# Performance work log

Hardware: AMD Instinct MI355X
Metric: run time of the kernel (lower is better)

The kernel has to match this reference:

```python
import jax, jax.numpy as jnp
import numpy as np

_OFF = [(dz, dy, dx) for dz in (-1, 0, 1) for dy in (-1, 0, 1) for dx in (-1, 0, 1)]
_K3 = [(kz, ky, kx) for kz in range(3) for ky in range(3) for kx in range(3)]


def _key(c, dims):
    D, H, W = dims
    return ((c[:, 0].astype(np.int64) * D + c[:, 1]) * H + c[:, 2]) * W + c[:, 3]


def _dedupe(c, dims):
    k = _key(c, dims)
    _, idx = np.unique(k, return_index=True)
    return c[np.sort(idx)]


def _make_lookup(coords, dims):
    D, H, W = dims
    keys = _key(coords, dims)
    order = np.argsort(keys)
    skeys = keys[order]

    def query(qc):
        valid = ((qc[:, 1] >= 0) & (qc[:, 1] < D) & (qc[:, 2] >= 0) & (qc[:, 2] < H)
                 & (qc[:, 3] >= 0) & (qc[:, 3] < W))
        qk = _key(np.where(valid[:, None], qc, 0), dims)
        pos = np.clip(np.searchsorted(skeys, qk), 0, len(skeys) - 1)
        hit = valid & (skeys[pos] == qk)
        return np.where(hit, order[pos], -1).astype(np.int32)
    return query


def _subm_nbr(coords, query):
    nbr = np.empty((len(coords), 27), np.int32)
    for ki, (dz, dy, dx) in enumerate(_OFF):
        qc = coords.copy()
        qc[:, 1] += dz; qc[:, 2] += dy; qc[:, 3] += dx
        nbr[:, ki] = query(qc)
    return nbr


def _down(in_coords, pads, out_dims, in_query):
    # spconv SparseConv3d k=3 s=2: output active set + gather rulebook (in = 2*out - p + k)
    p = np.array(pads)
    cand = []
    for k in _K3:
        t = in_coords[:, 1:] + p - np.array(k)
        m = (t % 2 == 0).all(1)
        o = t[m] // 2
        ok = (o >= 0).all(1) & (o < np.array(out_dims)).all(1)
        cand.append(np.concatenate([in_coords[m][ok][:, :1], o[ok]], 1))
    out_coords = _dedupe(np.concatenate(cand), out_dims)
    nbrd = np.empty((len(out_coords), 27), np.int32)
    for ki, k in enumerate(_K3):
        qc = out_coords.copy()
        qc[:, 1:] = out_coords[:, 1:] * 2 - p + np.array(k)
        nbrd[:, ki] = in_query(qc)
    return out_coords, nbrd


def _inv(in_coords, pads, out_query):
    # inverse conv: for each stride-s input voxel i, gather downsampled voxel o = (i+p-k)/2
    p = np.array(pads)
    nbr = np.full((len(in_coords), 27), -1, np.int32)
    for ki, k in enumerate(_K3):
        t = in_coords[:, 1:] + p - np.array(k)
        div = (t % 2 == 0).all(1)
        qc = in_coords.copy()
        qc[:, 1:] = np.where(div[:, None], t // 2, -1)
        nbr[:, ki] = np.where(div, out_query(qc), -1)
    return nbr


def setup_inputs() -> dict:
    rng = np.random.default_rng(0)
    B, K, P, STD = 4, 160, 128, 3.0
    D1 = (41, 1024, 1024)  # sparse_shape (z, y, x)
    pts = []
    for b in range(B):
        ctr = np.stack([rng.uniform(2, d - 3, K) for d in D1], 1)
        pb = ctr[:, None, :] + rng.normal(0.0, STD, (K, P, 3))
        pb = np.clip(np.rint(pb.reshape(-1, 3)), 0, np.array(D1) - 1).astype(np.int64)
        pts.append(np.concatenate([np.full((len(pb), 1), b, np.int64), pb], 1))
    c1 = _dedupe(np.concatenate(pts), D1)
    D2 = tuple((d + 2 * q - 3) // 2 + 1 for d, q in zip(D1, (1, 1, 1)))
    D3 = tuple((d + 2 * q - 3) // 2 + 1 for d, q in zip(D2, (1, 1, 1)))
    D4 = tuple((d + 2 * q - 3) // 2 + 1 for d, q in zip(D3, (0, 1, 1)))
    q1 = _make_lookup(c1, D1); nbr1 = _subm_nbr(c1, q1)
    c2, nbrd2 = _down(c1, (1, 1, 1), D2, q1); q2 = _make_lookup(c2, D2); nbr2 = _subm_nbr(c2, q2)
    c3, nbrd3 = _down(c2, (1, 1, 1), D3, q2); q3 = _make_lookup(c3, D3); nbr3 = _subm_nbr(c3, q3)
    c4, nbrd4 = _down(c3, (0, 1, 1), D4, q3); q4 = _make_lookup(c4, D4); nbr4 = _subm_nbr(c4, q4)
    nbri4 = _inv(c3, (0, 1, 1), q4)
    nbri3 = _inv(c2, (1, 1, 1), q3)
    nbri2 = _inv(c1, (1, 1, 1), q2)
    N1 = len(c1)
    w = lambda *s: jnp.asarray((0.05 * rng.standard_normal(s)).astype(np.float32))
    bn = lambda n, c: jnp.asarray(np.stack([1.0 + 0.02 * rng.standard_normal((n, c)),
                                            0.02 * rng.standard_normal((n, c))], 1).astype(np.float32))
    return {
        'voxel_feat': jnp.asarray(rng.standard_normal((N1, 4)).astype(np.float32)),
        'Win': w(27, 4, 32),
        'W32': w(10, 27, 32, 32),
        'W64': w(10, 27, 64, 64),
        'Wd3': w(27, 32, 64),
        'W6432': w(3, 27, 64, 32),
        'W12864': w(2, 27, 128, 64),
        'bn32': bn(14, 32),
        'bn64': bn(13, 64),
        'nbr1': jnp.asarray(nbr1), 'nbr2': jnp.asarray(nbr2),
        'nbr3': jnp.asarray(nbr3), 'nbr4': jnp.asarray(nbr4),
        'nbrd2': jnp.asarray(nbrd2), 'nbrd3': jnp.asarray(nbrd3), 'nbrd4': jnp.asarray(nbrd4),
        'nbri4': jnp.asarray(nbri4), 'nbri3': jnp.asarray(nbri3), 'nbri2': jnp.asarray(nbri2),
    }


def _conv(feat, nbr, W):
    # rulebook gather-matmul-scatter: out[n] = sum_k feat[nbr[n,k]] @ W[k]
    out = jnp.zeros((nbr.shape[0], W.shape[-1]), feat.dtype)
    for k in range(27):
        idx = nbr[:, k]
        g = jnp.where((idx >= 0)[:, None], feat[jnp.maximum(idx, 0)], 0.0)
        out = out + g @ W[k]
    return out


def _block(f, nbr, W, sb):  # conv + (folded, eval-mode) BN + ReLU
    return jax.nn.relu(_conv(f, nbr, W) * sb[0] + sb[1])


def _basic(f, nbr, Wa, sa, Wb, sb):  # SparseBasicBlock
    h = jax.nn.relu(_conv(f, nbr, Wa) * sa[0] + sa[1])
    h = _conv(h, nbr, Wb) * sb[0] + sb[1]
    return jax.nn.relu(h + f)


def _reduce(c, oc):  # channel_reduction: view(n, oc, -1).sum(2)
    return c.reshape(c.shape[0], oc, -1).sum(-1)


def _forward(voxel_feat, Win, W32, W64, Wd3, W6432, W12864, bn32, bn64,
             nbr1, nbr2, nbr3, nbr4, nbrd2, nbrd3, nbrd4, nbri4, nbri3, nbri2):
    x = _block(voxel_feat, nbr1, Win, bn32[0])       # conv_input
    x1 = _block(x, nbr1, W32[0], bn32[1])            # conv1
    h = _block(x1, nbrd2, W32[1], bn32[2])           # spconv2 stride-2
    h = _block(h, nbr2, W32[2], bn32[3])
    x2 = _block(h, nbr2, W32[3], bn32[4])
    h = _block(x2, nbrd3, Wd3, bn64[0])              # spconv3 stride-2, 32->64
    h = _block(h, nbr3, W64[0], bn64[1])
    x3 = _block(h, nbr3, W64[1], bn64[2])
    h = _block(x3, nbrd4, W64[2], bn64[3])           # spconv4 stride-2, pad (0,1,1)
    h = _block(h, nbr4, W64[3], bn64[4])
    x4 = _block(h, nbr4, W64[4], bn64[5])
    # UR block 4 (lateral = bottom = x4)
    t = _basic(x4, nbr4, W64[5], bn64[6], W64[6], bn64[7])
    cat = jnp.concatenate([x4, t], 1)                # [N4, 128]
    x = _block(cat, nbr4, W12864[0], bn64[11]) + _reduce(cat, 64)
    xu4 = _block(x, nbri4, W64[7], bn64[8])          # inverseconv -> level 3
    # UR block 3
    t = _basic(x3, nbr3, W64[8], bn64[9], W64[9], bn64[10])
    cat = jnp.concatenate([xu4, t], 1)
    x = _block(cat, nbr3, W12864[1], bn64[12]) + _reduce(cat, 64)
    xu3 = _block(x, nbri3, W6432[0], bn32[11])       # inverseconv -> level 2, 32ch
    # UR block 2
    t = _basic(x2, nbr2, W32[4], bn32[5], W32[5], bn32[6])
    cat = jnp.concatenate([xu3, t], 1)
    x = _block(cat, nbr2, W6432[1], bn32[12]) + _reduce(cat, 32)
    xu2 = _block(x, nbri2, W32[6], bn32[7])          # inverseconv -> level 1
    # UR block 1 (conv_inv = conv5, submanifold at level 1)
    t = _basic(x1, nbr1, W32[7], bn32[8], W32[8], bn32[9])
    cat = jnp.concatenate([xu2, t], 1)
    x = _block(cat, nbr1, W6432[2], bn32[13]) + _reduce(cat, 32)
    return _block(x, nbr1, W32[9], bn32[10])         # conv5 -> unet_voxel_feat [N1, 32]


def reference(voxel_feat, Win, W32, W64, Wd3, W6432, W12864, bn32, bn64,
              nbr1, nbr2, nbr3, nbr4, nbrd2, nbrd3, nbrd4, nbri4, nbri3, nbri2):
    return _forward(voxel_feat, Win, W32, W64, Wd3, W6432, W12864, bn32, bn64,
                    nbr1, nbr2, nbr3, nbr4, nbrd2, nbrd3, nbrd4, nbri4, nbri3, nbri2)
```

## Files before the change

kernel.cpp:

```cpp
#include <hip/hip_runtime.h>


typedef float f32x16 __attribute__((ext_vector_type(16)));

template<int CIN_A, int CIN_B, int COUT, int EPI, bool SPLIT>
__global__ __launch_bounds__(256) void spconv(
    const float* __restrict__ inA,
    const float* __restrict__ inB,
    const int*   __restrict__ nbr,
    const float* __restrict__ W,
    const float* __restrict__ bn,
    const float* __restrict__ skip,
    float*       __restrict__ out,
    float*       __restrict__ pout,
    int N, int KS)
{
    constexpr int CIN   = CIN_A + CIN_B;
    constexpr int CHUNK = (CIN >= 32) ? 32 : CIN;
    constexpr int NCHK  = CIN / CHUNK;
    constexpr int GV    = CHUNK / 4;
    constexpr int NSTEP = CHUNK * COUT / 64;

    const int tid = threadIdx.x;

    unsigned nwg = gridDim.x;
    unsigned q8 = nwg / 8u, r8 = nwg % 8u;
    unsigned xcd = blockIdx.x % 8u, sub = blockIdx.x / 8u;
    unsigned id = (xcd < r8 ? xcd * (q8 + 1u) : r8 * (q8 + 1u) + (xcd - r8) * q8) + sub;

    int kg, rb;
    if (SPLIT) { kg = (int)(id % (unsigned)KS); rb = (int)(id / (unsigned)KS); }
    else       { kg = 0;  rb = (int)id; }
    const int kper = SPLIT ? 27 / KS : 27;
    const int k0 = kg * kper, k1 = k0 + kper;

    const int  row = rb * 256 + tid;
    const bool rv  = row < N;
    const int* nbrp = nbr + (size_t)row * 27;

    float acc[COUT];
    #pragma unroll
    for (int i = 0; i < COUT; ++i) acc[i] = 0.f;

    int idx = rv ? nbrp[k0] : -1;
    for (int k = k0; k < k1; ++k) {
        const int nidx = (rv && k + 1 < k1) ? nbrp[k + 1] : -1;
        if (__ballot(idx >= 0) != 0ull) {
            const float mk = (idx >= 0) ? 1.f : 0.f;
            const int   si = (idx >= 0) ? idx : 0;
            const float* wk = W + (size_t)k * (CIN * COUT);

            #pragma unroll 1
            for (int c = 0; c < NCHK; ++c) {
                const float* src;
                if constexpr (CIN_B == 0)
                    src = inA + (size_t)si * CIN_A + c * CHUNK;
                else
                    src = (c * CHUNK < CIN_A)
                        ? inA + (size_t)si * CIN_A + c * CHUNK
                        : inB + (size_t)si * CIN_B + (c * CHUNK - CIN_A);
                float4 g[GV];
                #pragma unroll
                for (int v = 0; v < GV; ++v) g[v] = ((const float4*)src)[v];
                #pragma unroll
                for (int v = 0; v < GV; ++v) {
                    g[v].x *= mk; g[v].y *= mk; g[v].z *= mk; g[v].w *= mk;
                }

                const float* wkc = wk + c * (CHUNK * COUT);
                #pragma unroll
                for (int ss = 0; ss < NSTEP; ++ss) {
                    const float* wp = wkc + ss * 64;
                    f32x16 w0, w1, w2, w3;
                    asm volatile("s_load_dwordx16 %0, %1, 0x0"  : "=s"(w0) : "s"(wp));
                    asm volatile("s_load_dwordx16 %0, %1, 0x40" : "=s"(w1) : "s"(wp));
                    asm volatile("s_load_dwordx16 %0, %1, 0x80" : "=s"(w2) : "s"(wp));
                    asm volatile("s_load_dwordx16 %0, %1, 0xc0" : "=s"(w3) : "s"(wp));
                    asm volatile("s_waitcnt lgkmcnt(0)"
                                 : "+s"(w0), "+s"(w1), "+s"(w2), "+s"(w3));
                    if constexpr (COUT == 64) {
                        const int ci = ss;
                        const float gv = ((const float*)&g[ci >> 2])[ci & 3];
                        #pragma unroll
                        for (int q = 0; q < 16; ++q) acc[q]      += gv * w0[q];
                        #pragma unroll
                        for (int q = 0; q < 16; ++q) acc[16 + q] += gv * w1[q];
                        #pragma unroll
                        for (int q = 0; q < 16; ++q) acc[32 + q] += gv * w2[q];
                        #pragma unroll
                        for (int q = 0; q < 16; ++q) acc[48 + q] += gv * w3[q];
                    } else {
                        const int ci0 = 2 * ss, ci1 = 2 * ss + 1;
                        const float gv0 = ((const float*)&g[ci0 >> 2])[ci0 & 3];
                        const float gv1 = ((const float*)&g[ci1 >> 2])[ci1 & 3];
                        #pragma unroll
                        for (int q = 0; q < 16; ++q) acc[q]      += gv0 * w0[q];
                        #pragma unroll
                        for (int q = 0; q < 16; ++q) acc[16 + q] += gv0 * w1[q];
                        #pragma unroll
                        for (int q = 0; q < 16; ++q) acc[q]      += gv1 * w2[q];
                        #pragma unroll
                        for (int q = 0; q < 16; ++q) acc[16 + q] += gv1 * w3[q];
                    }
                }
            }
        }
        idx = nidx;
    }

    if (SPLIT) {
        if (rv) {
            float* pp = pout + ((size_t)kg * N + row) * COUT;
            #pragma unroll
            for (int q = 0; q < COUT / 4; ++q)
                *(float4*)(pp + q * 4) = make_float4(acc[4*q], acc[4*q+1], acc[4*q+2], acc[4*q+3]);
        }
        return;
    }
    if (!rv) return;

    float*       op   = out + (size_t)row * COUT;
    const float* skp  = (EPI == 1) ? skip + (size_t)row * COUT : nullptr;
    const float* catA = inA + (size_t)row * CIN_A;
    const float* catB = (CIN_B > 0) ? inB + (size_t)row * CIN_B : nullptr;

    #pragma unroll
    for (int q = 0; q < COUT / 4; ++q) {
        float4 sc = *(const float4*)(bn + q * 4);
        float4 bi = *(const float4*)(bn + COUT + q * 4);
        float4 y;
        y.x = acc[4*q+0] * sc.x + bi.x;
        y.y = acc[4*q+1] * sc.y + bi.y;
        y.z = acc[4*q+2] * sc.z + bi.z;
        y.w = acc[4*q+3] * sc.w + bi.w;
        if (EPI == 1) {
            float4 s = *(const float4*)(skp + q * 4);
            y.x += s.x; y.y += s.y; y.z += s.z; y.w += s.w;
        }
        y.x = fmaxf(y.x, 0.f); y.y = fmaxf(y.y, 0.f);
        y.z = fmaxf(y.z, 0.f); y.w = fmaxf(y.w, 0.f);
        if (EPI == 2) {
            const float* rs = (8 * q < CIN_A) ? catA + 8 * q : catB + 8 * q - CIN_A;
            float4 p0 = ((const float4*)rs)[0];
            float4 p1 = ((const float4*)rs)[1];
            y.x += p0.x + p0.y; y.y += p0.z + p0.w;
            y.z += p1.x + p1.y; y.w += p1.z + p1.w;
        }
        *(float4*)(op + q * 4) = y;
    }
}

template<int CIN_A, int CIN_B, int COUT, int EPI>
__global__ __launch_bounds__(256) void epi_k(
    const float* __restrict__ P, int KS,
    const float* __restrict__ bn,
    const float* __restrict__ skip,
    const float* __restrict__ inA,
    const float* __restrict__ inB,
    float* __restrict__ out, int N)
{
    int t = blockIdx.x * 256 + threadIdx.x;
    int total = N * (COUT / 4);
    if (t >= total) return;
    int r   = t / (COUT / 4);
    int co0 = (t % (COUT / 4)) * 4;

    float4 y = make_float4(0.f, 0.f, 0.f, 0.f);
    for (int kg = 0; kg < KS; ++kg) {
        float4 p = *(const float4*)(P + ((size_t)kg * N + r) * COUT + co0);
        y.x += p.x; y.y += p.y; y.z += p.z; y.w += p.w;
    }
    float4 sc = *(const float4*)(bn + co0);
    float4 bi = *(const float4*)(bn + COUT + co0);
    y.x = y.x * sc.x + bi.x; y.y = y.y * sc.y + bi.y;
    y.z = y.z * sc.z + bi.z; y.w = y.w * sc.w + bi.w;
    if (EPI == 1) {
        float4 s = *(const float4*)(skip + (size_t)r * COUT + co0);
        y.x += s.x; y.y += s.y; y.z += s.z; y.w += s.w;
    }
    y.x = fmaxf(y.x, 0.f); y.y = fmaxf(y.y, 0.f);
    y.z = fmaxf(y.z, 0.f); y.w = fmaxf(y.w, 0.f);
    if (EPI == 2) {
        const float* rs = (2 * co0 < CIN_A)
            ? inA + (size_t)r * CIN_A + 2 * co0
            : inB + (size_t)r * CIN_B + 2 * co0 - CIN_A;
        float4 p0 = ((const float4*)rs)[0];
        float4 p1 = ((const float4*)rs)[1];
        y.x += p0.x + p0.y; y.y += p0.z + p0.w;
        y.z += p1.x + p1.y; y.w += p1.z + p1.w;
    }
    *(float4*)(out + (size_t)r * COUT + co0) = y;
}

static inline int ksel(int nblk, int N, int CO, size_t prem_elems) {
    int ks = 27;
    if (nblk >= 640) ks = 1;
    else if (nblk * 3 >= 640) ks = 3;
    else if (nblk * 9 >= 640) ks = 9;
    while (ks > 1 && (size_t)ks * (size_t)N * (size_t)CO > prem_elems) ks /= 3;
    return ks;
}

extern "C" void kernel_launch(void* const* d_in, const int* in_sizes, int n_in,
                              void* d_out, int out_size, void* d_ws, size_t ws_size,
                              hipStream_t stream)
{
    (void)n_in; (void)out_size;
    const float* vf     = (const float*)d_in[0];
    const float* Win    = (const float*)d_in[1];
    const float* W32    = (const float*)d_in[2];
    const float* W64    = (const float*)d_in[3];
    const float* Wd3    = (const float*)d_in[4];
    const float* W6432  = (const float*)d_in[5];
    const float* W12864 = (const float*)d_in[6];
    const float* bn32   = (const float*)d_in[7];
    const float* bn64   = (const float*)d_in[8];
    const int* nbr1  = (const int*)d_in[9];
    const int* nbr2  = (const int*)d_in[10];
    const int* nbr3  = (const int*)d_in[11];
    const int* nbr4  = (const int*)d_in[12];
    const int* nbrd2 = (const int*)d_in[13];
    const int* nbrd3 = (const int*)d_in[14];
    const int* nbrd4 = (const int*)d_in[15];
    const int* nbri4 = (const int*)d_in[16];
    const int* nbri3 = (const int*)d_in[17];
    const int* nbri2 = (const int*)d_in[18];

    const int N1 = in_sizes[9]  / 27;
    const int N2 = in_sizes[10] / 27;
    const int N3 = in_sizes[11] / 27;
    const int N4 = in_sizes[12] / 27;

    float* ws = (float*)d_ws;
    size_t off = 0;
    auto alloc = [&](size_t n) { float* p = ws + off; off += n; return p; };
    float* X1  = alloc((size_t)N1 * 32);
    float* TA  = alloc((size_t)N1 * 32);
    float* TA2 = alloc((size_t)N1 * 32);
    float* TU1 = alloc((size_t)N1 * 32);
    float* X2  = alloc((size_t)N2 * 32);
    float* TB2 = alloc((size_t)N2 * 32);
    float* TC2 = alloc((size_t)N2 * 32);
    float* TU2 = alloc((size_t)N2 * 32);
    float* X3  = alloc((size_t)N3 * 64);
    float* TB3 = alloc((size_t)N3 * 64);
    float* TC3 = alloc((size_t)N3 * 64);
    float* TU3 = alloc((size_t)N3 * 64);
    float* X4  = alloc((size_t)N4 * 64);
    float* TB4 = alloc((size_t)N4 * 64);
    float* TC4 = alloc((size_t)N4 * 64);
    float* OUT = (float*)d_out;

    size_t prem = (ws_size / 4 > off + 1024) ? (ws_size / 4 - off - 1024) : 0;
    float* P = ws + off;

    const size_t S32 = 27*32*32, S64 = (size_t)27*64*64, S6432 = (size_t)27*64*32, S12864 = (size_t)27*128*64;

#define CONV(CA, CB, CO, EP, pA, pB, pN, pW, pBN, pS, pO, NN) do {                      \
        int nblk_ = ((NN) + 255) / 256;                                                 \
        int ks_ = ksel(nblk_, (NN), (CO), prem);                                        \
        if (ks_ == 1) {                                                                 \
            spconv<CA, CB, CO, EP, false><<<dim3((unsigned)nblk_), 256, 0, stream>>>(   \
                pA, pB, pN, pW, pBN, pS, pO, nullptr, NN, 1);                           \
        } else {                                                                        \
            spconv<CA, CB, CO, EP, true><<<dim3((unsigned)(nblk_ * ks_)), 256, 0, stream>>>( \
                pA, pB, pN, pW, pBN, pS, nullptr, P, NN, ks_);                          \
            int tot4_ = (NN) * ((CO) / 4);                                              \
            epi_k<CA, CB, CO, EP><<<dim3((unsigned)((tot4_ + 255) / 256)), 256, 0, stream>>>( \
                P, ks_, pBN, pS, pA, pB, pO, NN);                                       \
        }                                                                               \
    } while (0)

    CONV(4,0,32,0,  vf,  nullptr, nbr1,  Win,         bn32+0*64,  nullptr, TA,  N1);
    CONV(32,0,32,0, TA,  nullptr, nbr1,  W32+0*S32,   bn32+1*64,  nullptr, X1,  N1);
    CONV(32,0,32,0, X1,  nullptr, nbrd2, W32+1*S32,   bn32+2*64,  nullptr, TB2, N2);
    CONV(32,0,32,0, TB2, nullptr, nbr2,  W32+2*S32,   bn32+3*64,  nullptr, TC2, N2);
    CONV(32,0,32,0, TC2, nullptr, nbr2,  W32+3*S32,   bn32+4*64,  nullptr, X2,  N2);
    CONV(32,0,64,0, X2,  nullptr, nbrd3, Wd3,         bn64+0*128, nullptr, TB3, N3);
    CONV(64,0,64,0, TB3, nullptr, nbr3,  W64+0*S64,   bn64+1*128, nullptr, TC3, N3);
    CONV(64,0,64,0, TC3, nullptr, nbr3,  W64+1*S64,   bn64+2*128, nullptr, X3,  N3);
    CONV(64,0,64,0, X3,  nullptr, nbrd4, W64+2*S64,   bn64+3*128, nullptr, TB4, N4);
    CONV(64,0,64,0, TB4, nullptr, nbr4,  W64+3*S64,   bn64+4*128, nullptr, TC4, N4);
    CONV(64,0,64,0, TC4, nullptr, nbr4,  W64+4*S64,   bn64+5*128, nullptr, X4,  N4);
    CONV(64,0,64,0, X4,  nullptr, nbr4,  W64+5*S64,   bn64+6*128, nullptr, TB4, N4);
    CONV(64,0,64,1, TB4, nullptr, nbr4,  W64+6*S64,   bn64+7*128, X4,      TC4, N4);
    CONV(64,64,64,2, X4, TC4,     nbr4,  W12864+0*S12864, bn64+11*128, nullptr, TB4, N4);
    CONV(64,0,64,0, TB4, nullptr, nbri4, W64+7*S64,   bn64+8*128, nullptr, TU3, N3);
    CONV(64,0,64,0, X3,  nullptr, nbr3,  W64+8*S64,   bn64+9*128, nullptr, TB3, N3);
    CONV(64,0,64,1, TB3, nullptr, nbr3,  W64+9*S64,   bn64+10*128, X3,     TC3, N3);
    CONV(64,64,64,2, TU3, TC3,    nbr3,  W12864+1*S12864, bn64+12*128, nullptr, TB3, N3);
    CONV(64,0,32,0, TB3, nullptr, nbri3, W6432+0*S6432, bn32+11*64, nullptr, TU2, N2);
    CONV(32,0,32,0, X2,  nullptr, nbr2,  W32+4*S32,   bn32+5*64,  nullptr, TB2, N2);
    CONV(32,0,32,1, TB2, nullptr, nbr2,  W32+5*S32,   bn32+6*64,  X2,      TC2, N2);
    CONV(32,32,32,2, TU2, TC2,    nbr2,  W6432+1*S6432, bn32+12*64, nullptr, TB2, N2);
    CONV(32,0,32,0, TB2, nullptr, nbri2, W32+6*S32,   bn32+7*64,  nullptr, TU1, N1);
    CONV(32,0,32,0, X1,  nullptr, nbr1,  W32+7*S32,   bn32+8*64,  nullptr, TA,  N1);
    CONV(32,0,32,1, TA,  nullptr, nbr1,  W32+8*S32,   bn32+9*64,  X1,      TA2, N1);
    CONV(32,32,32,2, TU1, TA2,    nbr1,  W6432+2*S6432, bn32+13*64, nullptr, TA,  N1);
    CONV(32,0,32,0, TA,  nullptr, nbr1,  W32+9*S32,   bn32+10*64, nullptr, OUT, N1);
#undef CONV
}
```

Baseline: 4.438 ms.

## Split output channels across the four waves so each block covers 64 rows

```diff
diff --git a/kernel.cpp b/kernel.cpp
--- a/kernel.cpp
+++ b/kernel.cpp
@@ -2,6 +2,7 @@
 
 
 typedef float f32x16 __attribute__((ext_vector_type(16)));
+typedef float f32x8  __attribute__((ext_vector_type(8)));
 
 template<int CIN_A, int CIN_B, int COUT, int EPI, bool SPLIT>
 __global__ __launch_bounds__(256) void spconv(
@@ -16,12 +17,16 @@
     int N, int KS)
 {
     constexpr int CIN   = CIN_A + CIN_B;
+    constexpr int CPW   = COUT / 4;
     constexpr int CHUNK = (CIN >= 32) ? 32 : CIN;
     constexpr int NCHK  = CIN / CHUNK;
     constexpr int GV    = CHUNK / 4;
-    constexpr int NSTEP = CHUNK * COUT / 64;
-
-    const int tid = threadIdx.x;
+    constexpr int NB4   = CHUNK / 4;
+
+    const int tid  = threadIdx.x;
+    const int lane = tid & 63;
+    const int wid  = __builtin_amdgcn_readfirstlane(tid >> 6);
+    const int co0  = wid * CPW;
 
     unsigned nwg = gridDim.x;
     unsigned q8 = nwg / 8u, r8 = nwg % 8u;
@@ -34,13 +39,13 @@
     const int kper = SPLIT ? 27 / KS : 27;
     const int k0 = kg * kper, k1 = k0 + kper;
 
-    const int  row = rb * 256 + tid;
+    const int  row = rb * 64 + lane;
     const bool rv  = row < N;
     const int* nbrp = nbr + (size_t)row * 27;
 
-    float acc[COUT];
+    float acc[CPW];
     #pragma unroll
-    for (int i = 0; i < COUT; ++i) acc[i] = 0.f;
+    for (int i = 0; i < CPW; ++i) acc[i] = 0.f;
 
     int idx = rv ? nbrp[k0] : -1;
     for (int k = k0; k < k1; ++k) {
@@ -48,9 +53,9 @@
         if (__ballot(idx >= 0) != 0ull) {
             const float mk = (idx >= 0) ? 1.f : 0.f;
             const int   si = (idx >= 0) ? idx : 0;
-            const float* wk = W + (size_t)k * (CIN * COUT);
-
-            #pragma unroll 1
+            const float* wkb = W + (size_t)k * (CIN * COUT) + co0;
+
+            #pragma unroll
             for (int c = 0; c < NCHK; ++c) {
                 const float* src;
                 if constexpr (CIN_B == 0)
@@ -67,40 +72,46 @@
                     g[v].x *= mk; g[v].y *= mk; g[v].z *= mk; g[v].w *= mk;
                 }
 
-                const float* wkc = wk + c * (CHUNK * COUT);
+                const float* wp0 = wkb + (size_t)(c * CHUNK) * COUT;
                 #pragma unroll
-                for (int ss = 0; ss < NSTEP; ++ss) {
-                    const float* wp = wkc + ss * 64;
-                    f32x16 w0, w1, w2, w3;
-                    asm volatile("s_load_dwordx16 %0, %1, 0x0"  : "=s"(w0) : "s"(wp));
-                    asm volatile("s_load_dwordx16 %0, %1, 0x40" : "=s"(w1) : "s"(wp));
-                    asm volatile("s_load_dwordx16 %0, %1, 0x80" : "=s"(w2) : "s"(wp));
-                    asm volatile("s_load_dwordx16 %0, %1, 0xc0" : "=s"(w3) : "s"(wp));
-                    asm volatile("s_waitcnt lgkmcnt(0)"
-                                 : "+s"(w0), "+s"(w1), "+s"(w2), "+s"(w3));
+                for (int b = 0; b < NB4; ++b) {
+                    const float* wp = wp0 + (size_t)(4 * b) * COUT;
+                    const float g0 = (&g[b].x)[0];
+                    const float g1 = (&g[b].x)[1];
+                    const float g2 = (&g[b].x)[2];
+                    const float g3 = (&g[b].x)[3];
                     if constexpr (COUT == 64) {
-                        const int ci = ss;
-                        const float gv = ((const float*)&g[ci >> 2])[ci & 3];
-                        #pragma unroll
-                        for (int q = 0; q < 16; ++q) acc[q]      += gv * w0[q];
-                        #pragma unroll
-                        for (int q = 0; q < 16; ++q) acc[16 + q] += gv * w1[q];
-                        #pragma unroll
-                        for (int q = 0; q < 16; ++q) acc[32 + q] += gv * w2[q];
-                        #pragma unroll
-                        for (int q = 0; q < 16; ++q) acc[48 + q] += gv * w3[q];
+                        f32x16 w0, w1, w2, w3;
+                        asm volatile("s_load_dwordx16 %0, %1, 0x0"   : "=s"(w0) : "s"(wp));
+                        asm volatile("s_load_dwordx16 %0, %1, 0x100" : "=s"(w1) : "s"(wp));
+                        asm volatile("s_load_dwordx16 %0, %1, 0x200" : "=s"(w2) : "s"(wp));
+                        asm volatile("s_load_dwordx16 %0, %1, 0x300" : "=s"(w3) : "s"(wp));
+                        asm volatile("s_waitcnt lgkmcnt(0)"
+                                     : "+s"(w0), "+s"(w1), "+s"(w2), "+s"(w3));
+                        #pragma unroll
+                        for (int q = 0; q < 16; ++q) acc[q] += g0 * w0[q];
+                        #pragma unroll
+                        for (int q = 0; q < 16; ++q) acc[q] += g1 * w1[q];
+                        #pragma unroll
+                        for (int q = 0; q < 16; ++q) acc[q] += g2 * w2[q];
+                        #pragma unroll
+                        for (int q = 0; q < 16; ++q) acc[q] += g3 * w3[q];
                     } else {
-                        const int ci0 = 2 * ss, ci1 = 2 * ss + 1;
-                        const float gv0 = ((const float*)&g[ci0 >> 2])[ci0 & 3];
-                        const float gv1 = ((const float*)&g[ci1 >> 2])[ci1 & 3];
-                        #pragma unroll
-                        for (int q = 0; q < 16; ++q) acc[q]      += gv0 * w0[q];
-                        #pragma unroll
-                        for (int q = 0; q < 16; ++q) acc[16 + q] += gv0 * w1[q];
-                        #pragma unroll
-                        for (int q = 0; q < 16; ++q) acc[q]      += gv1 * w2[q];
-                        #pragma unroll
-                        for (int q = 0; q < 16; ++q) acc[16 + q] += gv1 * w3[q];
+                        f32x8 w0, w1, w2, w3;
+                        asm volatile("s_load_dwordx8 %0, %1, 0x0"   : "=s"(w0) : "s"(wp));
+                        asm volatile("s_load_dwordx8 %0, %1, 0x80"  : "=s"(w1) : "s"(wp));
+                        asm volatile("s_load_dwordx8 %0, %1, 0x100" : "=s"(w2) : "s"(wp));
+                        asm volatile("s_load_dwordx8 %0, %1, 0x180" : "=s"(w3) : "s"(wp));
+                        asm volatile("s_waitcnt lgkmcnt(0)"
+                                     : "+s"(w0), "+s"(w1), "+s"(w2), "+s"(w3));
+                        #pragma unroll
+                        for (int q = 0; q < 8; ++q) acc[q] += g0 * w0[q];
+                        #pragma unroll
+                        for (int q = 0; q < 8; ++q) acc[q] += g1 * w1[q];
+                        #pragma unroll
+                        for (int q = 0; q < 8; ++q) acc[q] += g2 * w2[q];
+                        #pragma unroll
+                        for (int q = 0; q < 8; ++q) acc[q] += g3 * w3[q];
                     }
                 }
             }
@@ -110,24 +121,25 @@
 
     if (SPLIT) {
         if (rv) {
-            float* pp = pout + ((size_t)kg * N + row) * COUT;
+            float* pp = pout + ((size_t)kg * N + row) * COUT + co0;
             #pragma unroll
-            for (int q = 0; q < COUT / 4; ++q)
-                *(float4*)(pp + q * 4) = make_float4(acc[4*q], acc[4*q+1], acc[4*q+2], acc[4*q+3]);
+            for (int q = 0; q < CPW / 4; ++q)
+                *(float4*)(pp + q * 4) =
+                    make_float4(acc[4*q], acc[4*q+1], acc[4*q+2], acc[4*q+3]);
         }
         return;
     }
     if (!rv) return;
 
-    float*       op   = out + (size_t)row * COUT;
-    const float* skp  = (EPI == 1) ? skip + (size_t)row * COUT : nullptr;
+    float*       op   = out + (size_t)row * COUT + co0;
+    const float* skp  = (EPI == 1) ? skip + (size_t)row * COUT + co0 : nullptr;
     const float* catA = inA + (size_t)row * CIN_A;
     const float* catB = (CIN_B > 0) ? inB + (size_t)row * CIN_B : nullptr;
 
     #pragma unroll
-    for (int q = 0; q < COUT / 4; ++q) {
-        float4 sc = *(const float4*)(bn + q * 4);
-        float4 bi = *(const float4*)(bn + COUT + q * 4);
+    for (int q = 0; q < CPW / 4; ++q) {
+        float4 sc = *(const float4*)(bn + co0 + q * 4);
+        float4 bi = *(const float4*)(bn + COUT + co0 + q * 4);
         float4 y;
         y.x = acc[4*q+0] * sc.x + bi.x;
         y.y = acc[4*q+1] * sc.y + bi.y;
@@ -140,7 +152,8 @@
         y.x = fmaxf(y.x, 0.f); y.y = fmaxf(y.y, 0.f);
         y.z = fmaxf(y.z, 0.f); y.w = fmaxf(y.w, 0.f);
         if (EPI == 2) {
-            const float* rs = (8 * q < CIN_A) ? catA + 8 * q : catB + 8 * q - CIN_A;
+            const int c2 = 2 * (co0 + 4 * q);
+            const float* rs = (c2 < CIN_A) ? catA + c2 : catB + c2 - CIN_A;
             float4 p0 = ((const float4*)rs)[0];
             float4 p1 = ((const float4*)rs)[1];
             y.x += p0.x + p0.y; y.y += p0.z + p0.w;
@@ -193,10 +206,10 @@
 }
 
 static inline int ksel(int nblk, int N, int CO, size_t prem_elems) {
-    int ks = 27;
-    if (nblk >= 640) ks = 1;
-    else if (nblk * 3 >= 640) ks = 3;
-    else if (nblk * 9 >= 640) ks = 9;
+    int ks;
+    if (nblk >= 1024) ks = 1;
+    else if (nblk * 3 >= 1024) ks = 3;
+    else ks = 9;
     while (ks > 1 && (size_t)ks * (size_t)N * (size_t)CO > prem_elems) ks /= 3;
     return ks;
 }
@@ -257,7 +270,7 @@
     const size_t S32 = 27*32*32, S64 = (size_t)27*64*64, S6432 = (size_t)27*64*32, S12864 = (size_t)27*128*64;
 
 #define CONV(CA, CB, CO, EP, pA, pB, pN, pW, pBN, pS, pO, NN) do {                      \
-        int nblk_ = ((NN) + 255) / 256;                                                 \
+        int nblk_ = ((NN) + 63) / 64;                                                   \
         int ks_ = ksel(nblk_, (NN), (CO), prem);                                        \
         if (ks_ == 1) {                                                                 \
             spconv<CA, CB, CO, EP, false><<<dim3((unsigned)nblk_), 256, 0, stream>>>(   \
```

Result: faster. 4.198 ms (-5.4%).
